# Performance work log

Measured on AMD Instinct MI355X. Metric: run time of the kernel, lower is better.

Reference implementation:

```python
import jax, jax.numpy as jnp
import numpy as np

TEMPERATURE = 0.5
EPS = 1e-8


def setup_inputs() -> dict:
    key = jax.random.key(0)
    k1, k2 = jax.random.split(key)
    B, D = 4096, 128
    z_i = jax.random.normal(k1, (B, D), dtype=jnp.float32)
    z_j = jax.random.normal(k2, (B, D), dtype=jnp.float32)
    return {"z_i": z_i, "z_j": z_j}


def reference(z_i, z_j):
    B = z_i.shape[0]
    N = 2 * B
    z = jnp.concatenate([z_i, z_j], axis=0)  # [N, D]
    # cosine similarity == normalize then Gram matrix (torch clamps denom by eps)
    norm = jnp.maximum(jnp.linalg.norm(z, axis=1, keepdims=True), EPS)
    zn = z / norm
    sim = (zn @ zn.T) / TEMPERATURE  # [N, N]
    # positive pairs sit on the +B / -B diagonals
    pos = jnp.concatenate([jnp.diagonal(sim, B), jnp.diagonal(sim, -B)])  # [N]
    # CE with label 0 over [pos | negatives(mask)] == logsumexp over all
    # non-self-diagonal entries minus the positive logit (pos re-enters the
    # logit row exactly once, so the union is: full row minus self-diagonal).
    neg_inf = jnp.asarray(-jnp.inf, dtype=sim.dtype)
    idx = jnp.arange(N)
    sim_masked = jnp.where(idx[:, None] == idx[None, :], neg_inf, sim)
    row_loss = jax.nn.logsumexp(sim_masked, axis=1) - pos  # [N]
    loss = jnp.sum(row_loss) / N  # CrossEntropyLoss(reduction='sum') / N
    return loss
```

## Files before the change

kernel.cpp:

```cpp
#include <hip/hip_runtime.h>
#include <hip/hip_bf16.h>

typedef __attribute__((ext_vector_type(8))) short short8;
typedef __attribute__((ext_vector_type(4))) float f32x4;
typedef __attribute__((address_space(1))) const unsigned int glb_u32;
typedef __attribute__((address_space(3))) unsigned int lds_u32;

#define DIMD 128
#define S 128
#define NS 64
#define NPB 32
#define WRW 32

#define ZSCALE 1.69864363f
#define LN2 0.6931471805599453f

__global__ __launch_bounds__(256) void nrm_kernel(const float* __restrict__ zi,
                                                  const float* __restrict__ zj,
                                                  __hip_bfloat16* __restrict__ zn,
                                                  float* __restrict__ out,
                                                  float* __restrict__ rowsum, int B) {
  if (blockIdx.x == 0 && threadIdx.x == 0) out[0] = 0.0f;
  int wave = threadIdx.x >> 6, lane = threadIdx.x & 63;
  int N = 2 * B;
  int row = blockIdx.x * 4 + wave;
  if (row >= N) return;
  if (lane == 0) rowsum[row] = 0.0f;
  const float* src = (row < B) ? (zi + (size_t)row * DIMD)
                               : (zj + (size_t)(row - B) * DIMD);
  float2 v = *(const float2*)(src + lane * 2);
  float ss = v.x * v.x + v.y * v.y;
  #pragma unroll
  for (int off = 32; off; off >>= 1) ss += __shfl_xor(ss, off);
  float nrm = sqrtf(ss);
  float r = ZSCALE / fmaxf(nrm, 1e-8f);
  __hip_bfloat16* dst = zn + (size_t)row * DIMD + lane * 2;
  dst[0] = __float2bfloat16(v.x * r);
  dst[1] = __float2bfloat16(v.y * r);
}


#define LDB(BB, SUB)                                                          \
  {                                                                           \
    const ushort* lp_ = &lds[((SUB) * 16 + l15) * DIMD];                      \
    _Pragma("unroll")                                                         \
    for (int kc = 0; kc < 4; ++kc) BB[kc] = *(const short8*)(lp_ + roff[kc]); \
  }

#define MM4(ACC, RG, BB)                                                      \
  ACC = __builtin_amdgcn_mfma_f32_16x16x32_bf16(a[RG][0], BB[0], ACC, 0, 0, 0); \
  ACC = __builtin_amdgcn_mfma_f32_16x16x32_bf16(a[RG][1], BB[1], ACC, 0, 0, 0); \
  ACC = __builtin_amdgcn_mfma_f32_16x16x32_bf16(a[RG][2], BB[2], ACC, 0, 0, 0); \
  ACC = __builtin_amdgcn_mfma_f32_16x16x32_bf16(a[RG][3], BB[3], ACC, 0, 0, 0);

#define EPI(ACC, RG, CE)                                                      \
  {                                                                           \
    float e0 = __builtin_amdgcn_exp2f(ACC[0]);                                \
    float e1 = __builtin_amdgcn_exp2f(ACC[1]);                                \
    float e2 = __builtin_amdgcn_exp2f(ACC[2]);                                \
    float e3 = __builtin_amdgcn_exp2f(ACC[3]);                                \
    rs[RG][0] += e0; rs[RG][1] += e1; rs[RG][2] += e2; rs[RG][3] += e3;       \
    CE += (e0 + e1) + (e2 + e3);                                              \
  }

#define CSTORE(CE, SUB)                                                       \
  {                                                                           \
    CE += __shfl_xor(CE, 16);                                                 \
    CE += __shfl_xor(CE, 32);                                                 \
    if (lh == 0) colred[wave][(SUB) * 16 + l15] = CE;                         \
  }

#define PAIR(S0, S1, PF0, PF1, DOPF)                                          \
  {                                                                           \
    f32x4 x0 = {0.f,0.f,0.f,0.f}, x1 = {0.f,0.f,0.f,0.f};                     \
    f32x4 y0 = {0.f,0.f,0.f,0.f}, y1 = {0.f,0.f,0.f,0.f};                     \
    MM4(x0, 0, b0) MM4(x1, 1, b0) MM4(y0, 0, b1) MM4(y1, 1, b1)               \
    if (DOPF) { LDB(b0, PF0) LDB(b1, PF1) }                                   \
    float ce0 = 0.f, ce1 = 0.f;                                               \
    EPI(x0, 0, ce0) EPI(x1, 1, ce0)                                           \
    EPI(y0, 0, ce1) EPI(y1, 1, ce1)                                           \
    CSTORE(ce0, S0) CSTORE(ce1, S1)                                           \
  }

__global__ __launch_bounds__(256) void sim_kernel(const __hip_bfloat16* __restrict__ znb,
                                                  float* __restrict__ rowsum,
                                                  float* __restrict__ pos, int B) {
  const ushort* zn = (const ushort*)znb;
  const int N = 2 * B;
  const int tid = threadIdx.x;
  const int wave = tid >> 6, lane = tid & 63;
  const int l15 = lane & 15, lh = lane >> 4;

  int rem = blockIdx.x, r = 0;
  while (rem >= (NS - r)) { rem -= (NS - r); ++r; }
  const int c = r + rem;

  const int Rr = r * S + wave * WRW;
  const int Cc = c * S;

  __shared__ ushort lds[S * DIMD];
  __shared__ float colred[4][S];

  {
    const int myCol = wave * 4 + lh;
    const int myKb = l15 ^ (myCol & 7);
    const ushort* gsrc0 = zn + (size_t)(Cc + myCol) * DIMD + myKb * 8;
    #pragma unroll
    for (int c_ = 0; c_ < 8; ++c_)
      __builtin_amdgcn_global_load_lds(
          (glb_u32*)(gsrc0 + (size_t)c_ * 16 * DIMD),
          (lds_u32*)&lds[(c_ * 16 + wave * 4) * DIMD], 16, 0, 0);
  }

  short8 a[2][4];
  #pragma unroll
  for (int rg = 0; rg < 2; ++rg) {
    const ushort* ar = zn + (size_t)(Rr + rg * 16 + l15) * DIMD + lh * 8;
    #pragma unroll
    for (int kc = 0; kc < 4; ++kc) a[rg][kc] = *(const short8*)(ar + kc * 32);
  }

  float rs[2][4];
  #pragma unroll
  for (int rg = 0; rg < 2; ++rg)
    #pragma unroll
    for (int rr = 0; rr < 4; ++rr) rs[rg][rr] = 0.0f;

  int roff[4];
  #pragma unroll
  for (int kc = 0; kc < 4; ++kc) roff[kc] = ((kc * 4 + lh) ^ (l15 & 7)) * 8;

  __syncthreads();

  if (r == c) {
    #pragma unroll 4
    for (int sub = 0; sub < S / 16; ++sub) {
      short8 bb[4];
      LDB(bb, sub)
      #pragma unroll
      for (int rg = 0; rg < 2; ++rg) {
        f32x4 acc = {0.f, 0.f, 0.f, 0.f};
        MM4(acc, rg, bb)
        #pragma unroll
        for (int rr = 0; rr < 4; ++rr) {
          int i_ = Rr + rg * 16 + lh * 4 + rr;
          int jg_ = Cc + sub * 16 + l15;
          if (jg_ != i_) rs[rg][rr] += __builtin_amdgcn_exp2f(acc[rr]);
        }
      }
    }
  } else if (c == r + NPB) {
    #pragma unroll 4
    for (int sub = 0; sub < S / 16; ++sub) {
      short8 bb[4];
      LDB(bb, sub)
      float ce = 0.0f;
      #pragma unroll
      for (int rg = 0; rg < 2; ++rg) {
        f32x4 acc = {0.f, 0.f, 0.f, 0.f};
        MM4(acc, rg, bb)
        #pragma unroll
        for (int rr = 0; rr < 4; ++rr) {
          int i_ = Rr + rg * 16 + lh * 4 + rr;
          int jg_ = Cc + sub * 16 + l15;
          float e = __builtin_amdgcn_exp2f(acc[rr]);
          rs[rg][rr] += e;
          ce += e;
          if (jg_ == i_ + B) {
            float s_ = acc[rr] * LN2;
            pos[i_] = s_;
            pos[i_ + B] = s_;
          }
        }
      }
      CSTORE(ce, sub)
    }
  } else {
    short8 b0[4], b1[4];
    LDB(b0, 0) LDB(b1, 1)
    PAIR(0, 1, 2, 3, 1)
    PAIR(2, 3, 4, 5, 1)
    PAIR(4, 5, 6, 7, 1)
    PAIR(6, 7, 0, 0, 0)
  }

  #pragma unroll
  for (int rg = 0; rg < 2; ++rg) {
    #pragma unroll
    for (int rr = 0; rr < 4; ++rr) {
      #pragma unroll
      for (int off = 1; off < 16; off <<= 1)
        rs[rg][rr] += __shfl_xor(rs[rg][rr], off);
    }
  }
  if (l15 == 0) {
    #pragma unroll
    for (int rg = 0; rg < 2; ++rg)
      #pragma unroll
      for (int rr = 0; rr < 4; ++rr)
        atomicAdd(&rowsum[Rr + rg * 16 + lh * 4 + rr], rs[rg][rr]);
  }

  if (r != c) {
    __syncthreads();
    if (tid < S) {
      float cs = colred[0][tid] + colred[1][tid] + colred[2][tid] + colred[3][tid];
      atomicAdd(&rowsum[Cc + tid], cs);
    }
  }
}

__global__ __launch_bounds__(256) void fin_kernel(const float* __restrict__ rowsum,
                                                  const float* __restrict__ pos,
                                                  float* __restrict__ out, int N) {
  int i = blockIdx.x * 256 + threadIdx.x;
  float li = 0.0f;
  if (i < N)
    li = __builtin_amdgcn_logf(rowsum[i]) * LN2 - pos[i];
  #pragma unroll
  for (int off = 32; off; off >>= 1) li += __shfl_xor(li, off);
  __shared__ float red[4];
  int wave = threadIdx.x >> 6, lane = threadIdx.x & 63;
  if (lane == 0) red[wave] = li;
  __syncthreads();
  if (threadIdx.x == 0) {
    float bs = red[0] + red[1] + red[2] + red[3];
    atomicAdd(out, bs / (float)N);
  }
}

extern "C" void kernel_launch(void* const* d_in, const int* in_sizes, int n_in,
                              void* d_out, int out_size, void* d_ws, size_t ws_size,
                              hipStream_t stream) {
  const float* zi = (const float*)d_in[0];
  const float* zj = (const float*)d_in[1];
  const int B = in_sizes[0] / DIMD;
  const int N = 2 * B;
  float* out = (float*)d_out;

  char* ws = (char*)d_ws;
  __hip_bfloat16* zn = (__hip_bfloat16*)ws;
  float* pos = (float*)(ws + (size_t)N * DIMD * 2);
  float* rowsum = (float*)(ws + (size_t)N * DIMD * 2 + (size_t)N * 4);

  nrm_kernel<<<N / 4, 256, 0, stream>>>(zi, zj, zn, out, rowsum, B);
  const int ntri = NS * (NS + 1) / 2;
  sim_kernel<<<ntri, 256, 0, stream>>>(zn, rowsum, pos, B);
  fin_kernel<<<N / 256, 256, 0, stream>>>(rowsum, pos, out, N);
}
```

Measured before the change: 38.58 us.

## Use 256x128 tiles in symmetric Gram sweep with strict-upper masking

Row tiles grow to 256 rows (64 per wave, four A fragments held in registers) against 128-column tiles, so each loaded B tile feeds twice as many MFMAs and fewer blocks are launched. Diagonal tiles now keep only strict upper-triangle entries and reuse the column-sum path, which removes the separate self-diagonal branch. The main loop becomes eight single-substep prefetch stages instead of paired substeps. The cost is higher register pressure and possibly lower occupancy, plus per-element compare masking on diagonal tiles.

```diff
diff --git a/kernel.cpp b/kernel.cpp
--- a/kernel.cpp
+++ b/kernel.cpp
@@ -7,10 +7,10 @@
 typedef __attribute__((address_space(3))) unsigned int lds_u32;
 
 #define DIMD 128
-#define S 128
-#define NS 64
-#define NPB 32
-#define WRW 32
+#define SR 256
+#define SC 128
+#define NR 32
+#define NC 64
 
 #define ZSCALE 1.69864363f
 #define LN2 0.6931471805599453f
@@ -53,7 +53,7 @@
   ACC = __builtin_amdgcn_mfma_f32_16x16x32_bf16(a[RG][2], BB[2], ACC, 0, 0, 0); \
   ACC = __builtin_amdgcn_mfma_f32_16x16x32_bf16(a[RG][3], BB[3], ACC, 0, 0, 0);
 
-#define EPI(ACC, RG, CE)                                                      \
+#define EPI_PLAIN(ACC, RG, CE, SUB)                                           \
   {                                                                           \
     float e0 = __builtin_amdgcn_exp2f(ACC[0]);                                \
     float e1 = __builtin_amdgcn_exp2f(ACC[1]);                                \
@@ -63,6 +63,32 @@
     CE += (e0 + e1) + (e2 + e3);                                              \
   }
 
+#define EPI_MASK(ACC, RG, CE, SUB)                                            \
+  {                                                                           \
+    _Pragma("unroll")                                                         \
+    for (int rr = 0; rr < 4; ++rr) {                                          \
+      int i_ = Rr + (RG) * 16 + lh * 4 + rr;                                  \
+      int jg_ = Cc + (SUB) * 16 + l15;                                        \
+      float e = (jg_ > i_) ? __builtin_amdgcn_exp2f(ACC[rr]) : 0.0f;          \
+      rs[RG][rr] += e; CE += e;                                               \
+    }                                                                         \
+  }
+
+#define EPI_POS(ACC, RG, CE, SUB)                                             \
+  {                                                                           \
+    _Pragma("unroll")                                                         \
+    for (int rr = 0; rr < 4; ++rr) {                                          \
+      int i_ = Rr + (RG) * 16 + lh * 4 + rr;                                  \
+      int jg_ = Cc + (SUB) * 16 + l15;                                        \
+      float e = __builtin_amdgcn_exp2f(ACC[rr]);                              \
+      rs[RG][rr] += e; CE += e;                                               \
+      if (jg_ == i_ + B) {                                                    \
+        float s_ = ACC[rr] * LN2;                                             \
+        pos[i_] = s_; pos[i_ + B] = s_;                                       \
+      }                                                                       \
+    }                                                                         \
+  }
+
 #define CSTORE(CE, SUB)                                                       \
   {                                                                           \
     CE += __shfl_xor(CE, 16);                                                 \
@@ -70,36 +96,51 @@
     if (lh == 0) colred[wave][(SUB) * 16 + l15] = CE;                         \
   }
 
-#define PAIR(S0, S1, PF0, PF1, DOPF)                                          \
-  {                                                                           \
-    f32x4 x0 = {0.f,0.f,0.f,0.f}, x1 = {0.f,0.f,0.f,0.f};                     \
-    f32x4 y0 = {0.f,0.f,0.f,0.f}, y1 = {0.f,0.f,0.f,0.f};                     \
-    MM4(x0, 0, b0) MM4(x1, 1, b0) MM4(y0, 0, b1) MM4(y1, 1, b1)               \
-    if (DOPF) { LDB(b0, PF0) LDB(b1, PF1) }                                   \
-    float ce0 = 0.f, ce1 = 0.f;                                               \
-    EPI(x0, 0, ce0) EPI(x1, 1, ce0)                                           \
-    EPI(y0, 0, ce1) EPI(y1, 1, ce1)                                           \
-    CSTORE(ce0, S0) CSTORE(ce1, S1)                                           \
+#define SUBSTEP(BCUR, BNXT, SUB, DOPF, EPIM)                                  \
+  {                                                                           \
+    if (DOPF) { LDB(BNXT, (SUB) + 1) }                                        \
+    float ce = 0.0f;                                                          \
+    _Pragma("unroll")                                                         \
+    for (int rg = 0; rg < 4; ++rg) {                                          \
+      f32x4 acc = {0.f, 0.f, 0.f, 0.f};                                       \
+      MM4(acc, rg, BCUR)                                                      \
+      EPIM(acc, rg, ce, SUB)                                                  \
+    }                                                                         \
+    CSTORE(ce, SUB)                                                           \
+  }
+
+#define RUN8(EPIM)                                                            \
+  {                                                                           \
+    short8 b0[4], b1[4];                                                      \
+    LDB(b0, 0)                                                                \
+    SUBSTEP(b0, b1, 0, 1, EPIM)                                               \
+    SUBSTEP(b1, b0, 1, 1, EPIM)                                               \
+    SUBSTEP(b0, b1, 2, 1, EPIM)                                               \
+    SUBSTEP(b1, b0, 3, 1, EPIM)                                               \
+    SUBSTEP(b0, b1, 4, 1, EPIM)                                               \
+    SUBSTEP(b1, b0, 5, 1, EPIM)                                               \
+    SUBSTEP(b0, b1, 6, 1, EPIM)                                               \
+    SUBSTEP(b1, b0, 7, 0, EPIM)                                               \
   }
 
 __global__ __launch_bounds__(256) void sim_kernel(const __hip_bfloat16* __restrict__ znb,
                                                   float* __restrict__ rowsum,
                                                   float* __restrict__ pos, int B) {
   const ushort* zn = (const ushort*)znb;
-  const int N = 2 * B;
   const int tid = threadIdx.x;
   const int wave = tid >> 6, lane = tid & 63;
   const int l15 = lane & 15, lh = lane >> 4;
 
   int rem = blockIdx.x, r = 0;
-  while (rem >= (NS - r)) { rem -= (NS - r); ++r; }
-  const int c = r + rem;
-
-  const int Rr = r * S + wave * WRW;
-  const int Cc = c * S;
-
-  __shared__ ushort lds[S * DIMD];
-  __shared__ float colred[4][S];
+  while (rem >= (NC - 2 * r)) { rem -= (NC - 2 * r); ++r; }
+  const int c = 2 * r + rem;
+  const int d = rem;
+
+  const int Rr = r * SR + wave * 64;
+  const int Cc = c * SC;
+
+  __shared__ ushort lds[SC * DIMD];
+  __shared__ float colred[4][SC];
 
   {
     const int myCol = wave * 4 + lh;
@@ -112,17 +153,17 @@
           (lds_u32*)&lds[(c_ * 16 + wave * 4) * DIMD], 16, 0, 0);
   }
 
-  short8 a[2][4];
-  #pragma unroll
-  for (int rg = 0; rg < 2; ++rg) {
+  short8 a[4][4];
+  #pragma unroll
+  for (int rg = 0; rg < 4; ++rg) {
     const ushort* ar = zn + (size_t)(Rr + rg * 16 + l15) * DIMD + lh * 8;
     #pragma unroll
     for (int kc = 0; kc < 4; ++kc) a[rg][kc] = *(const short8*)(ar + kc * 32);
   }
 
-  float rs[2][4];
-  #pragma unroll
-  for (int rg = 0; rg < 2; ++rg)
+  float rs[4][4];
+  #pragma unroll
+  for (int rg = 0; rg < 4; ++rg)
     #pragma unroll
     for (int rr = 0; rr < 4; ++rr) rs[rg][rr] = 0.0f;
 
@@ -132,60 +173,16 @@
 
   __syncthreads();
 
-  if (r == c) {
-    #pragma unroll 4
-    for (int sub = 0; sub < S / 16; ++sub) {
-      short8 bb[4];
-      LDB(bb, sub)
-      #pragma unroll
-      for (int rg = 0; rg < 2; ++rg) {
-        f32x4 acc = {0.f, 0.f, 0.f, 0.f};
-        MM4(acc, rg, bb)
-        #pragma unroll
-        for (int rr = 0; rr < 4; ++rr) {
-          int i_ = Rr + rg * 16 + lh * 4 + rr;
-          int jg_ = Cc + sub * 16 + l15;
-          if (jg_ != i_) rs[rg][rr] += __builtin_amdgcn_exp2f(acc[rr]);
-        }
-      }
-    }
-  } else if (c == r + NPB) {
-    #pragma unroll 4
-    for (int sub = 0; sub < S / 16; ++sub) {
-      short8 bb[4];
-      LDB(bb, sub)
-      float ce = 0.0f;
-      #pragma unroll
-      for (int rg = 0; rg < 2; ++rg) {
-        f32x4 acc = {0.f, 0.f, 0.f, 0.f};
-        MM4(acc, rg, bb)
-        #pragma unroll
-        for (int rr = 0; rr < 4; ++rr) {
-          int i_ = Rr + rg * 16 + lh * 4 + rr;
-          int jg_ = Cc + sub * 16 + l15;
-          float e = __builtin_amdgcn_exp2f(acc[rr]);
-          rs[rg][rr] += e;
-          ce += e;
-          if (jg_ == i_ + B) {
-            float s_ = acc[rr] * LN2;
-            pos[i_] = s_;
-            pos[i_ + B] = s_;
-          }
-        }
-      }
-      CSTORE(ce, sub)
-    }
+  if (d <= 1) {
+    RUN8(EPI_MASK)
+  } else if (d == 32 || d == 33) {
+    RUN8(EPI_POS)
   } else {
-    short8 b0[4], b1[4];
-    LDB(b0, 0) LDB(b1, 1)
-    PAIR(0, 1, 2, 3, 1)
-    PAIR(2, 3, 4, 5, 1)
-    PAIR(4, 5, 6, 7, 1)
-    PAIR(6, 7, 0, 0, 0)
-  }
-
-  #pragma unroll
-  for (int rg = 0; rg < 2; ++rg) {
+    RUN8(EPI_PLAIN)
+  }
+
+  #pragma unroll
+  for (int rg = 0; rg < 4; ++rg) {
     #pragma unroll
     for (int rr = 0; rr < 4; ++rr) {
       #pragma unroll
@@ -195,18 +192,16 @@
   }
   if (l15 == 0) {
     #pragma unroll
-    for (int rg = 0; rg < 2; ++rg)
+    for (int rg = 0; rg < 4; ++rg)
       #pragma unroll
       for (int rr = 0; rr < 4; ++rr)
         atomicAdd(&rowsum[Rr + rg * 16 + lh * 4 + rr], rs[rg][rr]);
   }
 
-  if (r != c) {
-    __syncthreads();
-    if (tid < S) {
-      float cs = colred[0][tid] + colred[1][tid] + colred[2][tid] + colred[3][tid];
-      atomicAdd(&rowsum[Cc + tid], cs);
-    }
+  __syncthreads();
+  if (tid < SC) {
+    float cs = colred[0][tid] + colred[1][tid] + colred[2][tid] + colred[3][tid];
+    atomicAdd(&rowsum[Cc + tid], cs);
   }
 }
 
@@ -244,7 +239,7 @@
   float* rowsum = (float*)(ws + (size_t)N * DIMD * 2 + (size_t)N * 4);
 
   nrm_kernel<<<N / 4, 256, 0, stream>>>(zi, zj, zn, out, rowsum, B);
-  const int ntri = NS * (NS + 1) / 2;
-  sim_kernel<<<ntri, 256, 0, stream>>>(zn, rowsum, pos, B);
+  const int ntiles = NR * NC - NR * (NR - 1);
+  sim_kernel<<<ntiles, 256, 0, stream>>>(zn, rowsum, pos, B);
   fin_kernel<<<N / 256, 256, 0, stream>>>(rowsum, pos, out, N);
 }
```

After: 54.66 us. +41.7%, slower.
